# Kernel tuning notes

Hardware: AMD Instinct MI355X
Metric: run time of the kernel (lower is better)

Reference implementation:

```python
import jax, jax.numpy as jnp
import numpy as np

B, N, D_S, D_A = 256, 200000, 96, 32
D = D_S + D_A
TIME_HORIZON = 1000
REWARD_SCALE = 5.0
REWARD_BANDWIDTH = 5.0 * TIME_HORIZON / np.sqrt(D)  # bandwidth_scale * T / sqrt(D)
TARGET_WEIGHT = 1.0 / TIME_HORIZON - 1e-6


def setup_inputs() -> dict:
    key = jax.random.key(0)
    k0, k1, k2, k3, k4 = jax.random.split(key, 5)
    state = jax.random.normal(k0, (B, D_S), jnp.float32)
    action = jax.random.normal(k1, (B, D_A), jnp.float32)
    expert_atoms = jax.random.normal(k2, (N, D), jnp.float32)
    expert_weights = jnp.full((N,), 1.0 / N, dtype=jnp.float32)
    scaler_mean = jax.random.normal(k3, (D,), jnp.float32) * 0.1
    scaler_std = jax.random.uniform(k4, (D,), jnp.float32, 0.5, 1.5)
    return {"state": state, "action": action, "expert_atoms": expert_atoms,
            "expert_weights": expert_weights, "scaler_mean": scaler_mean,
            "scaler_std": scaler_std}


def reference(state, action, expert_atoms, expert_weights, scaler_mean, scaler_std):
    # StandardScaler.transform on both agent atoms and expert atoms
    agent = (jnp.concatenate([state, action], axis=1) - scaler_mean) / scaler_std   # [B, D]
    experts = (expert_atoms - scaler_mean) / scaler_std                             # [N, D]
    # pairwise Euclidean distances via ||a||^2 + ||e||^2 - 2 a.e (avoids [B,N,D])
    a2 = jnp.sum(agent * agent, axis=-1)          # [B]
    e2 = jnp.sum(experts * experts, axis=-1)      # [N]
    d2 = a2[:, None] + e2[None, :] - 2.0 * (agent @ experts.T)  # [B, N]
    dists = jnp.sqrt(jnp.maximum(d2, 1e-12))
    # Greedy argmin weight-matching == consume mass in ascending-distance order:
    # sort + cumulative-weight threshold (single fused pass, no host syncs).
    order = jnp.argsort(dists, axis=1)                                # [B, N]
    d_sorted = jnp.take_along_axis(dists, order, axis=1)              # [B, N]
    w_sorted = expert_weights[order]                                  # [B, N]
    cum_prev = jnp.cumsum(w_sorted, axis=1) - w_sorted                # mass consumed before atom i
    take = jnp.clip(TARGET_WEIGHT - cum_prev, 0.0, w_sorted)          # mass taken from atom i
    cost = jnp.sum(take * d_sorted, axis=1)                           # [B]
    return REWARD_SCALE * jnp.exp(-REWARD_BANDWIDTH * cost)
```

## Files before the change

### kernel.cpp

```cpp
#include <hip/hip_runtime.h>
#include <hip/hip_bf16.h>
#include <hip/hip_fp16.h>

#define BATCH 256
#define NEXP 200000
#define DS 96
#define DA 32
#define DIM 128
#define NCHUNK 64
#define NBLK (NEXP / NCHUNK)
#define PREP_BLK 3125
#define SAMPLE_N 16384
#define SAMPLE_STRIDE 12
#define SCHUNK 32
#define SBLK (SAMPLE_N / SCHUNK)
#define SAMPLE_TARGET 64
#define MARGIN_BINS 4
#define TAU_BINS 2048
#define TAU_SCALE 16.0f
#define CAND_MAX 2048
#define STAGE_W 256
#define CNT_PAD 16
#define NGROUP 32
#define GSLOTS 128
#define HBINS 512
#define RBW 441.94173824159216

static __device__ __forceinline__ float target_w() { return (float)(1.0 / 1000.0 - 1e-6); }

typedef short short8v __attribute__((ext_vector_type(8)));
typedef float f32x4 __attribute__((ext_vector_type(4)));

#define OFF_EBF   0
#define OFF_E2    51200000
#define OFF_SD2   52000000
#define OFF_ABF   60388608
#define OFF_B2    60454144
#define OFF_THR   60455168
#define OFF_CNT2  60456192
#define OFF_CAND2 60980480
#define WS_NEEDED 65174784

__device__ __forceinline__ unsigned short f2bf(float x) {
    __hip_bfloat16 h = __float2bfloat16(x);
    return __builtin_bit_cast(unsigned short, h);
}

__device__ __forceinline__ void load_lds16(const void* g, void* l) {
    __builtin_amdgcn_global_load_lds(
        (const __attribute__((address_space(1))) unsigned int*)g,
        (__attribute__((address_space(3))) unsigned int*)l, 16, 0, 0);
}

__global__ __launch_bounds__(256) void k_prep(const float* __restrict__ experts,
                                              const float* __restrict__ stdv,
                                              const float* __restrict__ state,
                                              const float* __restrict__ action,
                                              unsigned short* __restrict__ ebf,
                                              float* __restrict__ e2g,
                                              unsigned short* __restrict__ agent_bf16,
                                              float* __restrict__ b2,
                                              int* __restrict__ cnt2) {
    __shared__ float rstdl[DIM];
    __shared__ float sq[64 * 33];
    int t = threadIdx.x, blk = blockIdx.x;
    int lane = t & 63, wave = t >> 6;
    if (t < DIM) rstdl[t] = 1.0f / stdv[t];
    __syncthreads();
    const float4* e4 = reinterpret_cast<const float4*>(experts) + (size_t)blk * 2048;
    ushort4* o4 = reinterpret_cast<ushort4*>(ebf) + (size_t)blk * 2048;
#pragma unroll
    for (int j = 0; j < 8; ++j) {
        int i4 = t + 256 * j;
        float4 v = e4[i4];
        int al = i4 >> 5, c32 = i4 & 31;
        int dbase = c32 * 4;
        float n0 = v.x * rstdl[dbase + 0];
        float n1 = v.y * rstdl[dbase + 1];
        float n2 = v.z * rstdl[dbase + 2];
        float n3 = v.w * rstdl[dbase + 3];
        sq[al * 33 + c32] = n0 * n0 + n1 * n1 + n2 * n2 + n3 * n3;
        ushort4 h; h.x = f2bf(n0); h.y = f2bf(n1); h.z = f2bf(n2); h.w = f2bf(n3);
        o4[i4] = h;
    }
    __syncthreads();
    if (t < 64) {
        float s = 0.f;
#pragma unroll
        for (int i = 0; i < 32; ++i) s += sq[t * 33 + i];
        e2g[blk * 64 + t] = s;
    }
    if (blk < BATCH) {
        __syncthreads();
        float rbb = 0.f;
        if (t < DIM) {
            float raw = (t < DS) ? state[blk * DS + t] : action[blk * DA + (t - DS)];
            float bb = raw * rstdl[t];
            agent_bf16[blk * DIM + t] = f2bf(bb);
            rbb = bb * bb;
        }
        if (t < NGROUP) cnt2[(blk * NGROUP + t) * CNT_PAD] = 0;
#pragma unroll
        for (int o = 32; o >= 1; o >>= 1) rbb += __shfl_xor(rbb, o, 64);
        if (lane == 0) sq[wave] = rbb;
        __syncthreads();
        if (t == 0) b2[blk] = sq[0] + sq[1] + sq[2] + sq[3];
    }
}

__global__ __launch_bounds__(256) void k_sample(const unsigned short* __restrict__ ebf,
                                                const float* __restrict__ e2g,
                                                const unsigned short* __restrict__ agent_bf16,
                                                const float* __restrict__ b2,
                                                _Float16* __restrict__ sd2) {
    __shared__ unsigned short elds[SCHUNK * DIM];
    __shared__ float e2l[SCHUNK];
    __shared__ float b2l[BATCH];

    int t = threadIdx.x, ci = blockIdx.x;
    int lane = t & 63, wave = t >> 6, quad = lane >> 4, lm = lane & 15;
    b2l[t] = b2[t];
    if (t < SCHUNK) e2l[t] = e2g[SAMPLE_STRIDE * (ci * SCHUNK + t)];

    {
        const char* gebf = (const char*)ebf;
        char* lbase = (char*)elds + wave * 2048;
#pragma unroll
        for (int q = 0; q < 2; ++q) {
            int aloc = wave * 8 + q * 4 + (lane >> 4);
            int atomg = SAMPLE_STRIDE * (ci * SCHUNK + aloc);
            int ch = (lane & 15) ^ (aloc & 15);
            load_lds16(gebf + (size_t)atomg * 256 + ch * 16, lbase + q * 1024);
        }
    }

    short8v afrag[4][4];
#pragma unroll
    for (int mt = 0; mt < 4; ++mt)
#pragma unroll
        for (int kk = 0; kk < 4; ++kk) {
            int row = wave * 64 + mt * 16 + lm;
            const uint4* p = reinterpret_cast<const uint4*>(agent_bf16 + row * DIM + kk * 32 + quad * 8);
            afrag[mt][kk] = __builtin_bit_cast(short8v, *p);
        }
    __syncthreads();

    f32x4 zero4 = {0.f, 0.f, 0.f, 0.f};
    f32x4 acc[4][2];
#pragma unroll
    for (int mt = 0; mt < 4; ++mt)
#pragma unroll
        for (int nt = 0; nt < 2; ++nt) acc[mt][nt] = zero4;
#pragma unroll
    for (int kk = 0; kk < 4; ++kk) {
        short8v bfrag[2];
#pragma unroll
        for (int nt = 0; nt < 2; ++nt) {
            int a = nt * 16 + lm;
            int ch = (kk * 4 + quad) ^ (a & 15);
            const uint4* p = reinterpret_cast<const uint4*>((const char*)elds + a * 256 + ch * 16);
            bfrag[nt] = __builtin_bit_cast(short8v, *p);
        }
#pragma unroll
        for (int mt = 0; mt < 4; ++mt)
#pragma unroll
            for (int nt = 0; nt < 2; ++nt)
                acc[mt][nt] = __builtin_amdgcn_mfma_f32_16x16x32_bf16(afrag[mt][kk], bfrag[nt], acc[mt][nt], 0, 0, 0);
    }

#pragma unroll
    for (int mt = 0; mt < 4; ++mt)
#pragma unroll
        for (int nt = 0; nt < 2; ++nt) {
            int atoml = nt * 16 + lm;
            float e2v = e2l[atoml];
#pragma unroll
            for (int r = 0; r < 4; ++r) {
                int row = wave * 64 + mt * 16 + quad * 4 + r;
                float d2 = b2l[row] + fmaf(-2.0f, acc[mt][nt][r], e2v);
                sd2[(size_t)row * SAMPLE_N + ci * SCHUNK + atoml] = (_Float16)d2;
            }
        }
}

__global__ __launch_bounds__(256) void k_tau(const _Float16* __restrict__ sd2,
                                             const float* __restrict__ b2,
                                             float* __restrict__ thr) {
    __shared__ unsigned int hist[TAU_BINS];
    __shared__ unsigned int part[256];
    int t = threadIdx.x, row = blockIdx.x;
    for (int i = t; i < TAU_BINS; i += 256) hist[i] = 0;
    __syncthreads();
    const uint4* r4 = reinterpret_cast<const uint4*>(sd2 + (size_t)row * SAMPLE_N);
#pragma unroll
    for (int it = 0; it < 8; ++it) {
        uint4 v = r4[t + 256 * it];
        unsigned int wv[4] = {v.x, v.y, v.z, v.w};
#pragma unroll
        for (int q = 0; q < 4; ++q)
#pragma unroll
            for (int hh = 0; hh < 2; ++hh) {
                unsigned short bits = (unsigned short)((wv[q] >> (16 * hh)) & 0xffffu);
                float d2f = (float)__builtin_bit_cast(_Float16, bits);
                int bn = (int)(sqrtf(fmaxf(d2f, 0.f)) * TAU_SCALE);
                bn = bn < 0 ? 0 : (bn > TAU_BINS - 1 ? TAU_BINS - 1 : bn);
                atomicAdd(&hist[bn], 1u);
            }
    }
    __syncthreads();
    unsigned int s = 0;
#pragma unroll
    for (int i = 0; i < 8; ++i) s += hist[t * 8 + i];
    part[t] = s;
    __syncthreads();
    if (t == 0) {
        unsigned int cum = 0;
        int B = TAU_BINS - 1;
        for (int c = 0; c < 256; ++c) {
            if (cum + part[c] >= SAMPLE_TARGET) {
                unsigned int cc = cum;
                for (int i = 0; i < 8; ++i) {
                    cc += hist[c * 8 + i];
                    if (cc >= SAMPLE_TARGET) { B = c * 8 + i; break; }
                }
                break;
            }
            cum += part[c];
        }
        int tb = B + MARGIN_BINS;
        if (tb > TAU_BINS - 1) tb = TAU_BINS - 1;
        float td = (float)(tb + 1) * (1.0f / TAU_SCALE);
        thr[row] = td * td - b2[row];
    }
}

__global__ __launch_bounds__(256, 4) void k_compact(const unsigned short* __restrict__ ebf,
                                                    const float* __restrict__ e2g,
                                                    const unsigned short* __restrict__ agent_bf16,
                                                    const float* __restrict__ thr,
                                                    const float* __restrict__ b2,
                                                    int* __restrict__ cnt2,
                                                    float* __restrict__ cand2) {
    __shared__ unsigned short elds[NCHUNK * DIM];
    __shared__ float e2l[NCHUNK];
    __shared__ float thrl[BATCH], b2l[BATCH];
    __shared__ unsigned int stage_rl[4][STAGE_W];
    __shared__ float stage_d2[4][STAGE_W];
    __shared__ int rowcnt[4][64], rowbase[4][64], rowoff[4][64];
    __shared__ int nlds[4][16];

    int t = threadIdx.x, chunkblk = blockIdx.x;
    int grp = chunkblk % NGROUP;
    int lane = t & 63, wave = t >> 6, quad = lane >> 4, lm = lane & 15;
    thrl[t] = thr[t];
    b2l[t] = b2[t];
    if (t < NCHUNK) e2l[t] = e2g[chunkblk * NCHUNK + t];
    rowcnt[wave][lane] = 0;
    rowoff[wave][lane] = 0;
    if (lane == 0) nlds[wave][0] = 0;

    {
        const char* gbase = (const char*)ebf + (size_t)chunkblk * NCHUNK * 256;
        char* lbase = (char*)elds + wave * 4096;
#pragma unroll
        for (int q = 0; q < 4; ++q) {
            int aloc = wave * 16 + q * 4 + (lane >> 4);
            int ch = (lane & 15) ^ (aloc & 15);
            load_lds16(gbase + (size_t)aloc * 256 + ch * 16, lbase + q * 1024);
        }
    }
    __syncthreads();

    f32x4 zero4 = {0.f, 0.f, 0.f, 0.f};
    f32x4 acc[4][4];
#pragma unroll
    for (int mt = 0; mt < 4; ++mt)
#pragma unroll
        for (int nt = 0; nt < 4; ++nt) acc[mt][nt] = zero4;

#pragma unroll
    for (int kk = 0; kk < 4; ++kk) {
        short8v afrag[4];
#pragma unroll
        for (int mt = 0; mt < 4; ++mt) {
            int row = wave * 64 + mt * 16 + lm;
            const uint4* p = reinterpret_cast<const uint4*>(agent_bf16 + row * DIM + kk * 32 + quad * 8);
            afrag[mt] = __builtin_bit_cast(short8v, *p);
        }
#pragma unroll
        for (int nt = 0; nt < 4; ++nt) {
            int a = nt * 16 + lm;
            int ch = (kk * 4 + quad) ^ (a & 15);
            const uint4* p = reinterpret_cast<const uint4*>((const char*)elds + a * 256 + ch * 16);
            short8v bfrag = __builtin_bit_cast(short8v, *p);
#pragma unroll
            for (int mt = 0; mt < 4; ++mt)
                acc[mt][nt] = __builtin_amdgcn_mfma_f32_16x16x32_bf16(afrag[mt], bfrag, acc[mt][nt], 0, 0, 0);
        }
    }

#pragma unroll
    for (int mt = 0; mt < 4; ++mt)
#pragma unroll
        for (int nt = 0; nt < 4; ++nt) {
            int atoml = nt * 16 + lm;
            float e2v = e2l[atoml];
#pragma unroll
            for (int r = 0; r < 4; ++r) {
                int rl = mt * 16 + quad * 4 + r;
                int row = wave * 64 + rl;
                float lhs = fmaf(-2.0f, acc[mt][nt][r], e2v);
                if (lhs <= thrl[row]) {
                    int p = atomicAdd(&nlds[wave][0], 1);
                    if (p < STAGE_W) {
                        stage_rl[wave][p] = (unsigned int)rl;
                        stage_d2[wave][p] = b2l[row] + lhs;
                        atomicAdd(&rowcnt[wave][rl], 1);
                    }
                }
            }
        }

    int n = nlds[wave][0];
    n = n < STAGE_W ? n : STAGE_W;

    int rc = rowcnt[wave][lane];
    if (rc > 0)
        rowbase[wave][lane] =
            atomicAdd(&cnt2[((wave * 64 + lane) * NGROUP + grp) * CNT_PAD], rc);

    for (int i = lane; i < n; i += 64) {
        int rl = (int)stage_rl[wave][i];
        int pos = rowbase[wave][rl] + atomicAdd(&rowoff[wave][rl], 1);
        if (pos < GSLOTS)
            cand2[((wave * 64 + rl) * NGROUP + grp) * GSLOTS + pos] = stage_d2[wave][i];
    }
}

__global__ __launch_bounds__(256) void k_cost(const float* __restrict__ cand2,
                                              const int* __restrict__ cnt2,
                                              const float* __restrict__ weights,
                                              const float* __restrict__ thr,
                                              const float* __restrict__ b2,
                                              float* __restrict__ out) {
    __shared__ float cdl[CAND_MAX];
    __shared__ unsigned int hist[HBINS];
    __shared__ unsigned int part[256];
    __shared__ int gcnt[NGROUP], goff[NGROUP + 1];
    __shared__ float bb[64];
    __shared__ float wred[4];
    __shared__ unsigned int wtot[4];
    __shared__ int nb;
    __shared__ int Bs, c0s;
    __shared__ float dmin2S;

    int t = threadIdx.x, row = blockIdx.x;
    int lane = t & 63, wave = t >> 6;
    for (int i = t; i < HBINS; i += 256) hist[i] = 0;
    if (t < NGROUP) {
        int nn = cnt2[(row * NGROUP + t) * CNT_PAD];
        gcnt[t] = nn < GSLOTS ? nn : GSLOTS;
    }
    if (t == 0) nb = 0;
    __syncthreads();
    if (t == 0) {
        int s = 0;
        for (int g = 0; g < NGROUP; ++g) { goff[g] = s; s += gcnt[g]; }
        goff[NGROUP] = s < CAND_MAX ? s : CAND_MAX;
    }
    __syncthreads();
    int nc = goff[NGROUP];
    float tau2 = thr[row] + b2[row];

    {
        for (int g = wave; g < NGROUP; g += 4) {
            int n = gcnt[g], base = goff[g];
            const float* src = cand2 + (row * NGROUP + g) * GSLOTS;
            for (int i = lane; i < n; i += 64) {
                int slot = base + i;
                if (slot < CAND_MAX) cdl[slot] = src[i];
            }
        }
    }
    __syncthreads();

    float mn = tau2;
    for (int i = t; i < nc; i += 256) mn = fminf(mn, cdl[i]);
#pragma unroll
    for (int o = 32; o >= 1; o >>= 1) mn = fminf(mn, __shfl_xor(mn, o, 64));
    if (lane == 0) wred[wave] = mn;
    __syncthreads();
    if (t == 0) dmin2S = fminf(fminf(wred[0], wred[1]), fminf(wred[2], wred[3]));
    __syncthreads();
    float dmin2 = dmin2S;
    float denom = tau2 - dmin2;
    float binscale = (float)HBINS / fmaxf(denom, 1e-12f);

    for (int i = t; i < nc; i += 256) {
        int bn = (int)((cdl[i] - dmin2) * binscale);
        bn = bn < 0 ? 0 : (bn > HBINS - 1 ? HBINS - 1 : bn);
        atomicAdd(&hist[bn], 1u);
    }
    __syncthreads();

    unsigned int pv = hist[2 * t] + hist[2 * t + 1];
    part[t] = pv;
    unsigned int inc = pv;
#pragma unroll
    for (int o = 1; o < 64; o <<= 1) {
        unsigned int up = __shfl_up(inc, o, 64);
        if (lane >= o) inc += up;
    }
    if (lane == 63) wtot[wave] = inc;
    __syncthreads();
    unsigned int woffs = 0;
    for (int w = 0; w < wave; ++w) woffs += wtot[w];
    unsigned int incl = inc + woffs;
    unsigned int before = incl - pv;
    if (before < 200u && incl >= 200u) {
        unsigned int h0 = hist[2 * t];
        if (before + h0 >= 200u) { Bs = 2 * t; c0s = (int)before; }
        else { Bs = 2 * t + 1; c0s = (int)(before + h0); }
    }
    __syncthreads();
    int B = Bs, c0 = c0s;

    float sloc = 0.f;
    for (int i = t; i < nc; i += 256) {
        float d2 = cdl[i];
        int bn = (int)((d2 - dmin2) * binscale);
        bn = bn < 0 ? 0 : (bn > HBINS - 1 ? HBINS - 1 : bn);
        if (bn < B) sloc += sqrtf(fmaxf(d2, 1e-12f));
        else if (bn == B) {
            int p = atomicAdd(&nb, 1);
            if (p < 64) bb[p] = sqrtf(fmaxf(d2, 1e-12f));
        }
    }
#pragma unroll
    for (int o = 32; o >= 1; o >>= 1) sloc += __shfl_xor(sloc, o, 64);
    if (lane == 0) wred[wave] = sloc;
    __syncthreads();

    if (t == 0) {
        float s0 = wred[0] + wred[1] + wred[2] + wred[3];
        int m = nb < 64 ? nb : 64;
        for (int i = 1; i < m; ++i) {
            float v = bb[i]; int j = i - 1;
            while (j >= 0 && bb[j] > v) { bb[j + 1] = bb[j]; --j; }
            bb[j + 1] = v;
        }
        int need = 200 - c0;
        if (need > m) need = m;
        float s199 = s0;
        for (int i = 0; i < need - 1; ++i) s199 += bb[i];
        float d200 = bb[need - 1];
        float w0 = weights[0];
        float cumw = 0.f;
        for (int i = 0; i < 199; ++i) cumw += w0;
        float TGT = target_w();
        float cost = w0 * s199 + (TGT - cumw) * d200;
        out[row] = 5.0f * expf(-(float)RBW * cost);
    }
}

extern "C" void kernel_launch(void* const* d_in, const int* in_sizes, int n_in,
                              void* d_out, int out_size, void* d_ws, size_t ws_size,
                              hipStream_t stream) {
    const float* state   = (const float*)d_in[0];
    const float* action  = (const float*)d_in[1];
    const float* experts = (const float*)d_in[2];
    const float* weights = (const float*)d_in[3];
    const float* stdv    = (const float*)d_in[5];
    float* out = (float*)d_out;

    if (ws_size < (size_t)WS_NEEDED) return;

    char* ws = (char*)d_ws;
    unsigned short* ebf        = (unsigned short*)(ws + OFF_EBF);
    float* e2g                 = (float*)(ws + OFF_E2);
    _Float16* sd2              = (_Float16*)(ws + OFF_SD2);
    unsigned short* agent_bf16 = (unsigned short*)(ws + OFF_ABF);
    float* b2                  = (float*)(ws + OFF_B2);
    float* thr                 = (float*)(ws + OFF_THR);
    int* cnt2                  = (int*)(ws + OFF_CNT2);
    float* cand2               = (float*)(ws + OFF_CAND2);

    k_prep<<<PREP_BLK, 256, 0, stream>>>(experts, stdv, state, action, ebf, e2g, agent_bf16, b2, cnt2);
    k_sample<<<SBLK, 256, 0, stream>>>(ebf, e2g, agent_bf16, b2, sd2);
    k_tau<<<BATCH, 256, 0, stream>>>(sd2, b2, thr);
    k_compact<<<NBLK, 256, 0, stream>>>(ebf, e2g, agent_bf16, thr, b2, cnt2, cand2);
    k_cost<<<BATCH, 256, 0, stream>>>(cand2, cnt2, weights, thr, b2, out);
}
```

Measured before the change: 240.0 us.

## Fuse expert normalization and bf16 conversion into sample and compact kernels

Removes the standalone prep pass that wrote a bf16 copy of all expert atoms plus their squared norms. Instead, k_sample and k_compact read raw fp32 experts, scale them by the inverse std, compute norms with shuffles, and write swizzled bf16 straight into LDS. A small k_agent kernel now handles agent normalization. This avoids writing and re-reading the 51MB bf16 buffer, but compact now reads fp32 (twice the bytes of bf16) and loses the async global-to-LDS loads.

```diff
diff --git a/kernel.cpp b/kernel.cpp
--- a/kernel.cpp
+++ b/kernel.cpp
@@ -9,7 +9,6 @@
 #define DIM 128
 #define NCHUNK 64
 #define NBLK (NEXP / NCHUNK)
-#define PREP_BLK 3125
 #define SAMPLE_N 16384
 #define SAMPLE_STRIDE 12
 #define SCHUNK 32
@@ -46,92 +45,73 @@
     return __builtin_bit_cast(unsigned short, h);
 }
 
-__device__ __forceinline__ void load_lds16(const void* g, void* l) {
-    __builtin_amdgcn_global_load_lds(
-        (const __attribute__((address_space(1))) unsigned int*)g,
-        (__attribute__((address_space(3))) unsigned int*)l, 16, 0, 0);
-}
-
-__global__ __launch_bounds__(256) void k_prep(const float* __restrict__ experts,
-                                              const float* __restrict__ stdv,
-                                              const float* __restrict__ state,
-                                              const float* __restrict__ action,
-                                              unsigned short* __restrict__ ebf,
-                                              float* __restrict__ e2g,
-                                              unsigned short* __restrict__ agent_bf16,
-                                              float* __restrict__ b2,
-                                              int* __restrict__ cnt2) {
-    __shared__ float rstdl[DIM];
-    __shared__ float sq[64 * 33];
-    int t = threadIdx.x, blk = blockIdx.x;
-    int lane = t & 63, wave = t >> 6;
-    if (t < DIM) rstdl[t] = 1.0f / stdv[t];
-    __syncthreads();
-    const float4* e4 = reinterpret_cast<const float4*>(experts) + (size_t)blk * 2048;
-    ushort4* o4 = reinterpret_cast<ushort4*>(ebf) + (size_t)blk * 2048;
-#pragma unroll
-    for (int j = 0; j < 8; ++j) {
-        int i4 = t + 256 * j;
-        float4 v = e4[i4];
-        int al = i4 >> 5, c32 = i4 & 31;
-        int dbase = c32 * 4;
-        float n0 = v.x * rstdl[dbase + 0];
-        float n1 = v.y * rstdl[dbase + 1];
-        float n2 = v.z * rstdl[dbase + 2];
-        float n3 = v.w * rstdl[dbase + 3];
-        sq[al * 33 + c32] = n0 * n0 + n1 * n1 + n2 * n2 + n3 * n3;
-        ushort4 h; h.x = f2bf(n0); h.y = f2bf(n1); h.z = f2bf(n2); h.w = f2bf(n3);
-        o4[i4] = h;
-    }
-    __syncthreads();
-    if (t < 64) {
-        float s = 0.f;
-#pragma unroll
-        for (int i = 0; i < 32; ++i) s += sq[t * 33 + i];
-        e2g[blk * 64 + t] = s;
-    }
-    if (blk < BATCH) {
+__device__ __forceinline__ unsigned int pk2bf(float a, float b) {
+    return (unsigned int)f2bf(a) | ((unsigned int)f2bf(b) << 16);
+}
+
+__global__ __launch_bounds__(128) void k_agent(const float* __restrict__ state,
+                                               const float* __restrict__ action,
+                                               const float* __restrict__ stdv,
+                                               unsigned short* __restrict__ agent_bf16,
+                                               float* __restrict__ b2,
+                                               int* __restrict__ cnt2) {
+    int b = blockIdx.x, d = threadIdx.x;
+    float raw = (d < DS) ? state[b * DS + d] : action[b * DA + (d - DS)];
+    float bb = raw / stdv[d];
+    agent_bf16[b * DIM + d] = f2bf(bb);
+    if (d < NGROUP) cnt2[(b * NGROUP + d) * CNT_PAD] = 0;
+    __shared__ float red[128];
+    red[d] = bb * bb;
+    __syncthreads();
+    for (int s = 64; s > 0; s >>= 1) {
+        if (d < s) red[d] += red[d + s];
         __syncthreads();
-        float rbb = 0.f;
-        if (t < DIM) {
-            float raw = (t < DS) ? state[blk * DS + t] : action[blk * DA + (t - DS)];
-            float bb = raw * rstdl[t];
-            agent_bf16[blk * DIM + t] = f2bf(bb);
-            rbb = bb * bb;
-        }
-        if (t < NGROUP) cnt2[(blk * NGROUP + t) * CNT_PAD] = 0;
-#pragma unroll
-        for (int o = 32; o >= 1; o >>= 1) rbb += __shfl_xor(rbb, o, 64);
-        if (lane == 0) sq[wave] = rbb;
-        __syncthreads();
-        if (t == 0) b2[blk] = sq[0] + sq[1] + sq[2] + sq[3];
-    }
-}
-
-__global__ __launch_bounds__(256) void k_sample(const unsigned short* __restrict__ ebf,
-                                                const float* __restrict__ e2g,
+    }
+    if (d == 0) b2[b] = red[0];
+}
+
+__global__ __launch_bounds__(256) void k_sample(const float* __restrict__ experts,
+                                                const float* __restrict__ stdv,
                                                 const unsigned short* __restrict__ agent_bf16,
                                                 const float* __restrict__ b2,
                                                 _Float16* __restrict__ sd2) {
-    __shared__ unsigned short elds[SCHUNK * DIM];
+    __shared__ __align__(16) unsigned short elds[SCHUNK * DIM];
     __shared__ float e2l[SCHUNK];
     __shared__ float b2l[BATCH];
+    __shared__ float rstdl[DIM];
 
     int t = threadIdx.x, ci = blockIdx.x;
     int lane = t & 63, wave = t >> 6, quad = lane >> 4, lm = lane & 15;
     b2l[t] = b2[t];
-    if (t < SCHUNK) e2l[t] = e2g[SAMPLE_STRIDE * (ci * SCHUNK + t)];
+    if (t < DIM) rstdl[t] = 1.0f / stdv[t];
+    __syncthreads();
 
     {
-        const char* gebf = (const char*)ebf;
-        char* lbase = (char*)elds + wave * 2048;
-#pragma unroll
-        for (int q = 0; q < 2; ++q) {
-            int aloc = wave * 8 + q * 4 + (lane >> 4);
-            int atomg = SAMPLE_STRIDE * (ci * SCHUNK + aloc);
-            int ch = (lane & 15) ^ (aloc & 15);
-            load_lds16(gebf + (size_t)atomg * 256 + ch * 16, lbase + q * 1024);
-        }
+        int al = t >> 3, p = t & 7;
+        int ag = SAMPLE_STRIDE * (ci * SCHUNK + al);
+        const float4* g4 = reinterpret_cast<const float4*>(experts + (size_t)ag * DIM + p * 16);
+        float4 v0 = g4[0], v1 = g4[1], v2 = g4[2], v3 = g4[3];
+        int db = p * 16;
+        float n0 = v0.x * rstdl[db + 0],  n1 = v0.y * rstdl[db + 1];
+        float n2 = v0.z * rstdl[db + 2],  n3 = v0.w * rstdl[db + 3];
+        float n4 = v1.x * rstdl[db + 4],  n5 = v1.y * rstdl[db + 5];
+        float n6 = v1.z * rstdl[db + 6],  n7 = v1.w * rstdl[db + 7];
+        float n8 = v2.x * rstdl[db + 8],  n9 = v2.y * rstdl[db + 9];
+        float na = v2.z * rstdl[db + 10], nb = v2.w * rstdl[db + 11];
+        float nc = v3.x * rstdl[db + 12], nd = v3.y * rstdl[db + 13];
+        float ne = v3.z * rstdl[db + 14], nf = v3.w * rstdl[db + 15];
+        float e2p = n0*n0 + n1*n1 + n2*n2 + n3*n3 + n4*n4 + n5*n5 + n6*n6 + n7*n7
+                  + n8*n8 + n9*n9 + na*na + nb*nb + nc*nc + nd*nd + ne*ne + nf*nf;
+        uint4 w0 = { pk2bf(n0, n1), pk2bf(n2, n3), pk2bf(n4, n5), pk2bf(n6, n7) };
+        uint4 w1 = { pk2bf(n8, n9), pk2bf(na, nb), pk2bf(nc, nd), pk2bf(ne, nf) };
+        int sw = al & 15;
+        uint4* lp = reinterpret_cast<uint4*>(elds);
+        lp[al * 16 + ((2 * p)     ^ sw)] = w0;
+        lp[al * 16 + ((2 * p + 1) ^ sw)] = w1;
+        e2p += __shfl_xor(e2p, 1, 64);
+        e2p += __shfl_xor(e2p, 2, 64);
+        e2p += __shfl_xor(e2p, 4, 64);
+        if (p == 0) e2l[al] = e2p;
     }
 
     short8v afrag[4][4];
@@ -234,16 +214,17 @@
     }
 }
 
-__global__ __launch_bounds__(256, 4) void k_compact(const unsigned short* __restrict__ ebf,
-                                                    const float* __restrict__ e2g,
+__global__ __launch_bounds__(256, 4) void k_compact(const float* __restrict__ experts,
+                                                    const float* __restrict__ stdv,
                                                     const unsigned short* __restrict__ agent_bf16,
                                                     const float* __restrict__ thr,
                                                     const float* __restrict__ b2,
                                                     int* __restrict__ cnt2,
                                                     float* __restrict__ cand2) {
-    __shared__ unsigned short elds[NCHUNK * DIM];
+    __shared__ __align__(16) unsigned short elds[NCHUNK * DIM];
     __shared__ float e2l[NCHUNK];
     __shared__ float thrl[BATCH], b2l[BATCH];
+    __shared__ float rstdl[DIM];
     __shared__ unsigned int stage_rl[4][STAGE_W];
     __shared__ float stage_d2[4][STAGE_W];
     __shared__ int rowcnt[4][64], rowbase[4][64], rowoff[4][64];
@@ -254,20 +235,34 @@
     int lane = t & 63, wave = t >> 6, quad = lane >> 4, lm = lane & 15;
     thrl[t] = thr[t];
     b2l[t] = b2[t];
-    if (t < NCHUNK) e2l[t] = e2g[chunkblk * NCHUNK + t];
+    if (t < DIM) rstdl[t] = 1.0f / stdv[t];
     rowcnt[wave][lane] = 0;
     rowoff[wave][lane] = 0;
     if (lane == 0) nlds[wave][0] = 0;
+    __syncthreads();
 
     {
-        const char* gbase = (const char*)ebf + (size_t)chunkblk * NCHUNK * 256;
-        char* lbase = (char*)elds + wave * 4096;
-#pragma unroll
-        for (int q = 0; q < 4; ++q) {
-            int aloc = wave * 16 + q * 4 + (lane >> 4);
-            int ch = (lane & 15) ^ (aloc & 15);
-            load_lds16(gbase + (size_t)aloc * 256 + ch * 16, lbase + q * 1024);
-        }
+        int al = t >> 2, p = t & 3;
+        const float4* g4 = reinterpret_cast<const float4*>(
+            experts + ((size_t)(chunkblk * NCHUNK + al)) * DIM + p * 32);
+        float e2p = 0.f;
+        int sw = al & 15;
+        uint4* lp = reinterpret_cast<uint4*>(elds);
+#pragma unroll
+        for (int k = 0; k < 4; ++k) {
+            float4 a = g4[2 * k], b = g4[2 * k + 1];
+            int db = p * 32 + k * 8;
+            float m0 = a.x * rstdl[db + 0], m1 = a.y * rstdl[db + 1];
+            float m2 = a.z * rstdl[db + 2], m3 = a.w * rstdl[db + 3];
+            float m4 = b.x * rstdl[db + 4], m5 = b.y * rstdl[db + 5];
+            float m6 = b.z * rstdl[db + 6], m7 = b.w * rstdl[db + 7];
+            e2p += m0*m0 + m1*m1 + m2*m2 + m3*m3 + m4*m4 + m5*m5 + m6*m6 + m7*m7;
+            uint4 w = { pk2bf(m0, m1), pk2bf(m2, m3), pk2bf(m4, m5), pk2bf(m6, m7) };
+            lp[al * 16 + ((p * 4 + k) ^ sw)] = w;
+        }
+        e2p += __shfl_xor(e2p, 1, 64);
+        e2p += __shfl_xor(e2p, 2, 64);
+        if (p == 0) e2l[al] = e2p;
     }
     __syncthreads();
 
@@ -476,8 +471,6 @@
     if (ws_size < (size_t)WS_NEEDED) return;
 
     char* ws = (char*)d_ws;
-    unsigned short* ebf        = (unsigned short*)(ws + OFF_EBF);
-    float* e2g                 = (float*)(ws + OFF_E2);
     _Float16* sd2              = (_Float16*)(ws + OFF_SD2);
     unsigned short* agent_bf16 = (unsigned short*)(ws + OFF_ABF);
     float* b2                  = (float*)(ws + OFF_B2);
@@ -485,9 +478,9 @@
     int* cnt2                  = (int*)(ws + OFF_CNT2);
     float* cand2               = (float*)(ws + OFF_CAND2);
 
-    k_prep<<<PREP_BLK, 256, 0, stream>>>(experts, stdv, state, action, ebf, e2g, agent_bf16, b2, cnt2);
-    k_sample<<<SBLK, 256, 0, stream>>>(ebf, e2g, agent_bf16, b2, sd2);
+    k_agent<<<BATCH, 128, 0, stream>>>(state, action, stdv, agent_bf16, b2, cnt2);
+    k_sample<<<SBLK, 256, 0, stream>>>(experts, stdv, agent_bf16, b2, sd2);
     k_tau<<<BATCH, 256, 0, stream>>>(sd2, b2, thr);
-    k_compact<<<NBLK, 256, 0, stream>>>(ebf, e2g, agent_bf16, thr, b2, cnt2, cand2);
+    k_compact<<<NBLK, 256, 0, stream>>>(experts, stdv, agent_bf16, thr, b2, cnt2, cand2);
     k_cost<<<BATCH, 256, 0, stream>>>(cand2, cnt2, weights, thr, b2, out);
 }
```

Result: faster. 222.1 us (-7.5%).
